# Kernel tuning notes

Measured on AMD Instinct MI355X. Metric: run time of the kernel, lower is better.

Reference implementation:

```python
import jax, jax.numpy as jnp
import numpy as np

D_MODEL = 512
WINDOW = 128
N_HEADS = 8


def setup_inputs() -> dict:
    key = jax.random.key(0)
    k1, k2, k3, k4, k5 = jax.random.split(key, 5)
    B, S, D = 8, 4096, D_MODEL
    scale = 1.0 / np.sqrt(D)
    return {
        "x": jax.random.normal(k1, (B, S, D), dtype=jnp.float32),
        "in_proj_w": jax.random.normal(k2, (3 * D, D), dtype=jnp.float32) * scale,
        "in_proj_b": jax.random.normal(k3, (3 * D,), dtype=jnp.float32) * 0.02,
        "out_proj_w": jax.random.normal(k4, (D, D), dtype=jnp.float32) * scale,
        "out_proj_b": jax.random.normal(k5, (D,), dtype=jnp.float32) * 0.02,
    }


def reference(x, in_proj_w, in_proj_b, out_proj_w, out_proj_b):
    # Non-overlapping sliding-window MHA with shared weights per window.
    B, S, D = x.shape
    W = WINDOW
    H = N_HEADS
    hd = D // H
    nw = S // W  # S chosen divisible by window size

    xw = x.reshape(B, nw, W, D)
    # Fused QKV projection (torch in_proj_weight layout: [3D, D], y = x @ W^T + b)
    qkv = jnp.einsum("bnwd,ed->bnwe", xw, in_proj_w) + in_proj_b  # [B,nw,W,3D]
    q, k, v = jnp.split(qkv, 3, axis=-1)

    def to_heads(t):
        return t.reshape(B, nw, W, H, hd)

    q = to_heads(q) * (1.0 / np.sqrt(hd))
    k = to_heads(k)
    v = to_heads(v)

    # Block-diagonal attention: scores only within each window [B,nw,H,W,W]
    scores = jnp.einsum("bnqhd,bnkhd->bnhqk", q, k)
    attn = jax.nn.softmax(scores, axis=-1)
    ctx = jnp.einsum("bnhqk,bnkhd->bnqhd", attn, v)  # [B,nw,W,H,hd]
    ctx = ctx.reshape(B, S, D)

    out = jnp.einsum("bsd,ed->bse", ctx, out_proj_w) + out_proj_b
    return out
```

## Files before the change

### kernel.cpp

```cpp
#include <hip/hip_runtime.h>


typedef __bf16 bf16x8 __attribute__((ext_vector_type(8)));
typedef __bf16 bf16x4 __attribute__((ext_vector_type(4)));
typedef float  f32x4  __attribute__((ext_vector_type(4)));

#define MFMA16(a, b, c) __builtin_amdgcn_mfma_f32_16x16x32_bf16((a), (b), (c), 0, 0, 0)

#define VMCNT_(n) asm volatile("s_waitcnt vmcnt(" #n ")" ::: "memory")
#define VMCNT(n) VMCNT_(n)
#define LGKM0() asm volatile("s_waitcnt lgkmcnt(0)" ::: "memory")

__device__ __forceinline__ void gload_lds16(const __bf16* g, void* l) {
    __builtin_amdgcn_global_load_lds(
        (const __attribute__((address_space(1))) unsigned int*)g,
        (__attribute__((address_space(3))) unsigned int*)l, 16, 0, 0);
}

__device__ __forceinline__ void cvt8(const float* __restrict__ s,
                                     __bf16* __restrict__ d, long i) {
    const float4* s4 = reinterpret_cast<const float4*>(s);
    float4 a = s4[2 * i], b = s4[2 * i + 1];
    bf16x8 v;
    v[0] = (__bf16)a.x; v[1] = (__bf16)a.y; v[2] = (__bf16)a.z; v[3] = (__bf16)a.w;
    v[4] = (__bf16)b.x; v[5] = (__bf16)b.y; v[6] = (__bf16)b.z; v[7] = (__bf16)b.w;
    *reinterpret_cast<bf16x8*>(d + 8 * i) = v;
}

__global__ void convert_k(const float* __restrict__ x,
                          const float* __restrict__ w_in,
                          const float* __restrict__ w_out,
                          __bf16* __restrict__ x_bf,
                          __bf16* __restrict__ w_in_bf,
                          __bf16* __restrict__ w_out_bf)
{
    long i0 = (long)blockIdx.x * blockDim.x + threadIdx.x;
    long stride = (long)gridDim.x * blockDim.x;
    for (long i = i0; i < 16777216 / 8; i += stride) cvt8(x, x_bf, i);
    for (long i = i0; i < 786432 / 8;   i += stride) cvt8(w_in, w_in_bf, i);
    for (long i = i0; i < 262144 / 8;   i += stride) cvt8(w_out, w_out_bf, i);
}

template<int EPI, int NN>
__global__ __launch_bounds__(512, 2)
void gemm256(const __bf16* __restrict__ A,
             const __bf16* __restrict__ Bw,
             const float* __restrict__ bias,
             void* __restrict__ Cq,
             __bf16* __restrict__ vT)
{
    __shared__ __bf16 Al[4][8192];
    __shared__ __bf16 Bl[4][8192];

    const int nwg = gridDim.x;
    const int chunk = nwg >> 3;
    const int bid = blockIdx.x;
    const int wg = (bid & 7) * chunk + (bid >> 3);
    const int nidx = wg % NN;
    const int midx = wg / NN;
    const long mbase = (long)midx * 256;
    const int colbase = nidx * 256;

    const int tid = threadIdx.x;
    const int w = tid >> 6, lane = tid & 63;
    const int lrow = lane & 15, hi = lane >> 4;
    const int wm = w >> 2, wn = w & 3;

    const int st_row = lane >> 2;
    const int st_k = 8 * ((lane & 3) ^ ((lane >> 3) & 3));
    const int rd_off = 16 * (hi ^ ((lrow >> 1) & 3));

    const __bf16* PA = A  + (mbase + w * 16 + st_row) * 512 + st_k;
    const __bf16* PB = Bw + ((long)colbase + w * 16 + st_row) * 512 + st_k;
    const int lds_w = w * 1024;

    f32x4 acc[8][4];
    #pragma unroll
    for (int rt = 0; rt < 8; ++rt)
        #pragma unroll
        for (int ct = 0; ct < 4; ++ct) acc[rt][ct] = (f32x4){0.f, 0.f, 0.f, 0.f};

    auto stage = [&](int tt) {
        const int kk = tt * 32;
        char* As = (char*)Al[tt & 3];
        char* Bs = (char*)Bl[tt & 3];
        gload_lds16(PA + kk,             As + lds_w);
        gload_lds16(PA + 128 * 512 + kk, As + 8192 + lds_w);
        gload_lds16(PB + kk,             Bs + lds_w);
        gload_lds16(PB + 128 * 512 + kk, Bs + 8192 + lds_w);
    };

#define ITER(T, VM, DO_STG)                                                       \
    {                                                                             \
        VMCNT(VM);                                                                \
        LGKM0();                                                                  \
        __builtin_amdgcn_s_barrier();                                             \
        if (DO_STG) stage((T) + 3);                                               \
        const char* As = (const char*)Al[(T) & 3];                                \
        const char* Bs = (const char*)Bl[(T) & 3];                                \
        bf16x8 af[8], bfr[4];                                                     \
        _Pragma("unroll")                                                         \
        for (int rt = 0; rt < 8; ++rt) {                                          \
            int row = 128 * wm + 16 * rt + lrow;                                  \
            af[rt] = *reinterpret_cast<const bf16x8*>(As + row * 64 + rd_off);    \
        }                                                                         \
        _Pragma("unroll")                                                         \
        for (int ct = 0; ct < 4; ++ct) {                                          \
            int row = 64 * wn + 16 * ct + lrow;                                   \
            bfr[ct] = *reinterpret_cast<const bf16x8*>(Bs + row * 64 + rd_off);   \
        }                                                                         \
        __builtin_amdgcn_s_setprio(1);                                            \
        _Pragma("unroll")                                                         \
        for (int rt = 0; rt < 8; ++rt)                                            \
            _Pragma("unroll")                                                     \
            for (int ct = 0; ct < 4; ++ct)                                        \
                acc[rt][ct] = MFMA16(af[rt], bfr[ct], acc[rt][ct]);               \
        __builtin_amdgcn_s_setprio(0);                                            \
    }

    stage(0); stage(1); stage(2);

    #pragma unroll 1
    for (int t = 0; t < 13; ++t) ITER(t, 8, 1);
    ITER(13, 8, 0);
    ITER(14, 4, 0);
    ITER(15, 0, 0);
#undef ITER

    if (EPI == 0) {
        const int region = colbase >> 9;
        if (region < 2) {
            __bf16* qk = (__bf16*)Cq;
            const float scale = (region == 0) ? 0.125f : 1.0f;
            #pragma unroll
            for (int ct = 0; ct < 4; ++ct) {
                int colg = colbase + 64 * wn + 16 * ct + lrow;
                float b = bias[colg];
                #pragma unroll
                for (int rt = 0; rt < 8; ++rt) {
                    long row = mbase + 128 * wm + 16 * rt + 4 * hi;
                    #pragma unroll
                    for (int r = 0; r < 4; ++r)
                        qk[(row + r) * 1024 + colg] = (__bf16)((acc[rt][ct][r] + b) * scale);
                }
            }
        } else {
            #pragma unroll
            for (int ct = 0; ct < 4; ++ct) {
                int colg = colbase + 64 * wn + 16 * ct + lrow;
                float b = bias[colg];
                int e2 = colg - 1024;
                int h = e2 >> 6, d = e2 & 63;
                #pragma unroll
                for (int rt = 0; rt < 8; ++rt) {
                    long row = mbase + 128 * wm + 16 * rt + 4 * hi;
                    int win = (int)(row >> 7), tok0 = (int)(row & 127);
                    bf16x4 pk;
                    pk[0] = (__bf16)(acc[rt][ct][0] + b);
                    pk[1] = (__bf16)(acc[rt][ct][1] + b);
                    pk[2] = (__bf16)(acc[rt][ct][2] + b);
                    pk[3] = (__bf16)(acc[rt][ct][3] + b);
                    *reinterpret_cast<bf16x4*>(
                        vT + (((long)win * 8 + h) * 64 + d) * 128 + tok0) = pk;
                }
            }
        }
    } else {
        float* out = (float*)Cq;
        #pragma unroll
        for (int ct = 0; ct < 4; ++ct) {
            int colg = colbase + 64 * wn + 16 * ct + lrow;
            float b = bias[colg];
            #pragma unroll
            for (int rt = 0; rt < 8; ++rt) {
                long row = mbase + 128 * wm + 16 * rt + 4 * hi;
                #pragma unroll
                for (int r = 0; r < 4; ++r)
                    out[(row + r) * 512 + colg] = acc[rt][ct][r] + b;
            }
        }
    }
}

__global__ __launch_bounds__(256)
void swa_attn(const __bf16* __restrict__ qk,
              const __bf16* __restrict__ vT,
              __bf16* __restrict__ ctx)
{
    __shared__ __bf16 p_lds[4][32][136];

    const int bid = blockIdx.x;
    const int win = bid >> 3, h = bid & 7;
    const int tid = threadIdx.x;
    const int w = tid >> 6, lane = tid & 63;
    const int lrow = lane & 15, hi = lane >> 4;
    const long tokb = (long)win * 128;

    bf16x8 qa[2][2];
    #pragma unroll
    for (int rt = 0; rt < 2; ++rt)
        #pragma unroll
        for (int ks = 0; ks < 2; ++ks)
            qa[rt][ks] = *reinterpret_cast<const bf16x8*>(
                qk + (tokb + 32 * w + 16 * rt + lrow) * 1024 + h * 64 + ks * 32 + hi * 8);

    f32x4 s[2][8];
    #pragma unroll
    for (int rt = 0; rt < 2; ++rt)
        #pragma unroll
        for (int ct = 0; ct < 8; ++ct) s[rt][ct] = (f32x4){0.f, 0.f, 0.f, 0.f};
    #pragma unroll
    for (int ks = 0; ks < 2; ++ks) {
        #pragma unroll
        for (int ct = 0; ct < 8; ++ct) {
            bf16x8 kb = *reinterpret_cast<const bf16x8*>(
                qk + (tokb + 16 * ct + lrow) * 1024 + 512 + h * 64 + ks * 32 + hi * 8);
            s[0][ct] = MFMA16(qa[0][ks], kb, s[0][ct]);
            s[1][ct] = MFMA16(qa[1][ks], kb, s[1][ct]);
        }
    }

    float inv[2][4];
    #pragma unroll
    for (int rt = 0; rt < 2; ++rt) {
        #pragma unroll
        for (int r = 0; r < 4; ++r) {
            float m = s[rt][0][r];
            #pragma unroll
            for (int ct = 1; ct < 8; ++ct) m = fmaxf(m, s[rt][ct][r]);
            m = fmaxf(m, __shfl_xor(m, 1));
            m = fmaxf(m, __shfl_xor(m, 2));
            m = fmaxf(m, __shfl_xor(m, 4));
            m = fmaxf(m, __shfl_xor(m, 8));
            float sum = 0.f;
            #pragma unroll
            for (int ct = 0; ct < 8; ++ct) {
                float e = __expf(s[rt][ct][r] - m);
                sum += e;
                p_lds[w][16 * rt + 4 * hi + r][16 * ct + lrow] = (__bf16)e;
            }
            sum += __shfl_xor(sum, 1);
            sum += __shfl_xor(sum, 2);
            sum += __shfl_xor(sum, 4);
            sum += __shfl_xor(sum, 8);
            inv[rt][r] = 1.f / sum;
        }
    }

    f32x4 o[2][4];
    #pragma unroll
    for (int rt = 0; rt < 2; ++rt)
        #pragma unroll
        for (int ct = 0; ct < 4; ++ct) o[rt][ct] = (f32x4){0.f, 0.f, 0.f, 0.f};
    const __bf16* vb = vT + ((long)win * 8 + h) * 64 * 128;
    #pragma unroll
    for (int kt = 0; kt < 4; ++kt) {
        bf16x8 pa0 = *reinterpret_cast<const bf16x8*>(&p_lds[w][lrow][32 * kt + 8 * hi]);
        bf16x8 pa1 = *reinterpret_cast<const bf16x8*>(&p_lds[w][16 + lrow][32 * kt + 8 * hi]);
        #pragma unroll
        for (int ct = 0; ct < 4; ++ct) {
            bf16x8 vf = *reinterpret_cast<const bf16x8*>(
                vb + (16 * ct + lrow) * 128 + 32 * kt + 8 * hi);
            o[0][ct] = MFMA16(pa0, vf, o[0][ct]);
            o[1][ct] = MFMA16(pa1, vf, o[1][ct]);
        }
    }

    #pragma unroll
    for (int rt = 0; rt < 2; ++rt)
        #pragma unroll
        for (int ct = 0; ct < 4; ++ct)
            #pragma unroll
            for (int r = 0; r < 4; ++r) {
                long tok = tokb + 32 * w + 16 * rt + 4 * hi + r;
                ctx[tok * 512 + h * 64 + 16 * ct + lrow] =
                    (__bf16)(o[rt][ct][r] * inv[rt][r]);
            }
}

extern "C" void kernel_launch(void* const* d_in, const int* in_sizes, int n_in,
                              void* d_out, int out_size, void* d_ws, size_t ws_size,
                              hipStream_t stream)
{
    const float* x     = (const float*)d_in[0];
    const float* w_in  = (const float*)d_in[1];
    const float* b_in  = (const float*)d_in[2];
    const float* w_out = (const float*)d_in[3];
    const float* b_out = (const float*)d_in[4];

    char* ws = (char*)d_ws;
    __bf16* x_bf     = (__bf16*)(ws);
    __bf16* ctx      = (__bf16*)(ws);
    __bf16* vT       = (__bf16*)(ws + 33554432);
    __bf16* w_in_bf  = (__bf16*)(ws + 67108864);
    __bf16* w_out_bf = (__bf16*)(ws + 68681728);
    __bf16* qk       = (__bf16*)d_out;

    convert_k<<<2048, 256, 0, stream>>>(x, w_in, w_out, x_bf, w_in_bf, w_out_bf);
    gemm256<0, 6><<<768, 512, 0, stream>>>(x_bf, w_in_bf, b_in, (void*)qk, vT);
    swa_attn<<<2048, 256, 0, stream>>>(qk, vT, ctx);
    gemm256<1, 2><<<256, 512, 0, stream>>>(ctx, w_out_bf, b_out, d_out, nullptr);
}
```

Measured before the change: 176.3 us.

## Restructure GEMM to BK=64 double-buffered pipeline with LDS-staged coalesced epilogues

Reworks the 256x256 GEMM main loop: K tiles grow from 32 to 64 with two LDS buffers instead of four. Each tile is split into four barrier-separated sub-phases that reuse the B fragments across A row groups, with a new XOR swizzle layout. All epilogues now stage results through LDS so global writes to qk, the transposed vT and the fp32 output are 16-byte coalesced vectors. This trades extra barriers and less prefetch depth (one tile ahead, then full vmcnt(0) waits) for fewer loop iterations, fewer registers and better store coalescing.

```diff
diff --git a/kernel.cpp b/kernel.cpp
--- a/kernel.cpp
+++ b/kernel.cpp
@@ -2,7 +2,6 @@
 
 
 typedef __bf16 bf16x8 __attribute__((ext_vector_type(8)));
-typedef __bf16 bf16x4 __attribute__((ext_vector_type(4)));
 typedef float  f32x4  __attribute__((ext_vector_type(4)));
 
 #define MFMA16(a, b, c) __builtin_amdgcn_mfma_f32_16x16x32_bf16((a), (b), (c), 0, 0, 0)
@@ -49,8 +48,7 @@
              void* __restrict__ Cq,
              __bf16* __restrict__ vT)
 {
-    __shared__ __bf16 Al[4][8192];
-    __shared__ __bf16 Bl[4][8192];
+    __shared__ __align__(16) char smem[131072];
 
     const int nwg = gridDim.x;
     const int chunk = nwg >> 3;
@@ -64,15 +62,28 @@
     const int tid = threadIdx.x;
     const int w = tid >> 6, lane = tid & 63;
     const int lrow = lane & 15, hi = lane >> 4;
+    const int quad = lane >> 4, sl = lane & 15;
     const int wm = w >> 2, wn = w & 3;
 
-    const int st_row = lane >> 2;
-    const int st_k = 8 * ((lane & 3) ^ ((lane >> 3) & 3));
-    const int rd_off = 16 * (hi ^ ((lrow >> 1) & 3));
-
-    const __bf16* PA = A  + (mbase + w * 16 + st_row) * 512 + st_k;
-    const __bf16* PB = Bw + ((long)colbase + w * 16 + st_row) * 512 + st_k;
-    const int lds_w = w * 1024;
+    const int l8 = lane >> 3;
+    const int slotp = (lane & 7) ^ l8;
+    const __bf16* stA = A  + (mbase + 8 * w + l8) * 512 + slotp * 8;
+    const __bf16* stB = Bw + ((long)colbase + 8 * w + l8) * 512 + slotp * 8;
+    const int ldsw = w * 1024;
+
+    auto stage8 = [&](int tt) {
+        char* As = smem + (tt & 1) * 32768;
+        char* Bs = smem + 65536 + (tt & 1) * 32768;
+        const int ko = tt * 64;
+        gload_lds16(stA + ko,             As + ldsw);
+        gload_lds16(stA + 64 * 512 + ko,  As + 8192 + ldsw);
+        gload_lds16(stA + 128 * 512 + ko, As + 16384 + ldsw);
+        gload_lds16(stA + 192 * 512 + ko, As + 24576 + ldsw);
+        gload_lds16(stB + ko,             Bs + ldsw);
+        gload_lds16(stB + 64 * 512 + ko,  Bs + 8192 + ldsw);
+        gload_lds16(stB + 128 * 512 + ko, Bs + 16384 + ldsw);
+        gload_lds16(stB + 192 * 512 + ko, Bs + 24576 + ldsw);
+    };
 
     f32x4 acc[8][4];
     #pragma unroll
@@ -80,104 +91,152 @@
         #pragma unroll
         for (int ct = 0; ct < 4; ++ct) acc[rt][ct] = (f32x4){0.f, 0.f, 0.f, 0.f};
 
-    auto stage = [&](int tt) {
-        const int kk = tt * 32;
-        char* As = (char*)Al[tt & 3];
-        char* Bs = (char*)Bl[tt & 3];
-        gload_lds16(PA + kk,             As + lds_w);
-        gload_lds16(PA + 128 * 512 + kk, As + 8192 + lds_w);
-        gload_lds16(PB + kk,             Bs + lds_w);
-        gload_lds16(PB + 128 * 512 + kk, Bs + 8192 + lds_w);
-    };
-
-#define ITER(T, VM, DO_STG)                                                       \
+    bf16x8 af[4], bfr[4];
+
+#define PHASE(T, KK, RT0, LB)                                                     \
     {                                                                             \
-        VMCNT(VM);                                                                \
-        LGKM0();                                                                  \
-        __builtin_amdgcn_s_barrier();                                             \
-        if (DO_STG) stage((T) + 3);                                               \
-        const char* As = (const char*)Al[(T) & 3];                                \
-        const char* Bs = (const char*)Bl[(T) & 3];                                \
-        bf16x8 af[8], bfr[4];                                                     \
-        _Pragma("unroll")                                                         \
-        for (int rt = 0; rt < 8; ++rt) {                                          \
-            int row = 128 * wm + 16 * rt + lrow;                                  \
-            af[rt] = *reinterpret_cast<const bf16x8*>(As + row * 64 + rd_off);    \
+        const char* As = smem + ((T) & 1) * 32768;                                \
+        const char* Bs = smem + 65536 + ((T) & 1) * 32768;                        \
+        const int ko = ((KK) * 64 + hi * 16) ^ ((lrow & 7) << 4);                 \
+        if (LB) {                                                                 \
+            _Pragma("unroll")                                                     \
+            for (int ct = 0; ct < 4; ++ct)                                        \
+                bfr[ct] = *reinterpret_cast<const bf16x8*>(                       \
+                    Bs + (64 * wn + 16 * ct + lrow) * 128 + ko);                  \
         }                                                                         \
         _Pragma("unroll")                                                         \
-        for (int ct = 0; ct < 4; ++ct) {                                          \
-            int row = 64 * wn + 16 * ct + lrow;                                   \
-            bfr[ct] = *reinterpret_cast<const bf16x8*>(Bs + row * 64 + rd_off);   \
-        }                                                                         \
+        for (int i = 0; i < 4; ++i)                                               \
+            af[i] = *reinterpret_cast<const bf16x8*>(                             \
+                As + (128 * wm + 16 * ((RT0) + i) + lrow) * 128 + ko);            \
         __builtin_amdgcn_s_setprio(1);                                            \
         _Pragma("unroll")                                                         \
-        for (int rt = 0; rt < 8; ++rt)                                            \
+        for (int i = 0; i < 4; ++i)                                               \
             _Pragma("unroll")                                                     \
             for (int ct = 0; ct < 4; ++ct)                                        \
-                acc[rt][ct] = MFMA16(af[rt], bfr[ct], acc[rt][ct]);               \
+                acc[(RT0) + i][ct] = MFMA16(af[i], bfr[ct], acc[(RT0) + i][ct]);  \
         __builtin_amdgcn_s_setprio(0);                                            \
     }
 
-    stage(0); stage(1); stage(2);
+    stage8(0); stage8(1);
+    VMCNT(8);
+    __builtin_amdgcn_s_barrier();
 
     #pragma unroll 1
-    for (int t = 0; t < 13; ++t) ITER(t, 8, 1);
-    ITER(13, 8, 0);
-    ITER(14, 4, 0);
-    ITER(15, 0, 0);
-#undef ITER
-
+    for (int t = 0; t < 8; ++t) {
+        if (t) {
+            VMCNT(0);
+            __builtin_amdgcn_s_barrier();
+            if (t < 7) stage8(t + 1);
+        }
+        PHASE(t, 0, 0, 1);
+        __builtin_amdgcn_s_barrier();
+        PHASE(t, 0, 4, 0);
+        __builtin_amdgcn_s_barrier();
+        PHASE(t, 1, 0, 1);
+        __builtin_amdgcn_s_barrier();
+        PHASE(t, 1, 4, 0);
+    }
+#undef PHASE
+    __builtin_amdgcn_s_barrier();
+
+    const int colg0 = colbase + 64 * wn + lrow;
     if (EPI == 0) {
-        const int region = colbase >> 9;
-        if (region < 2) {
+        if (colbase < 1024) {
+            const float scale = (colbase < 512) ? 0.125f : 1.0f;
             __bf16* qk = (__bf16*)Cq;
-            const float scale = (region == 0) ? 0.125f : 1.0f;
             #pragma unroll
             for (int ct = 0; ct < 4; ++ct) {
-                int colg = colbase + 64 * wn + 16 * ct + lrow;
-                float b = bias[colg];
-                #pragma unroll
-                for (int rt = 0; rt < 8; ++rt) {
-                    long row = mbase + 128 * wm + 16 * rt + 4 * hi;
+                float b = bias[colg0 + 16 * ct];
+                int col2 = (64 * wn + 16 * ct + lrow) * 2;
+                #pragma unroll
+                for (int rt = 0; rt < 8; ++rt)
                     #pragma unroll
-                    for (int r = 0; r < 4; ++r)
-                        qk[(row + r) * 1024 + colg] = (__bf16)((acc[rt][ct][r] + b) * scale);
+                    for (int r = 0; r < 4; ++r) {
+                        int row = 128 * wm + 16 * rt + 4 * hi + r;
+                        *reinterpret_cast<__bf16*>(
+                            smem + row * 512 + (col2 ^ ((row & 31) << 4))) =
+                            (__bf16)((acc[rt][ct][r] + b) * scale);
+                    }
+            }
+            LGKM0();
+            __builtin_amdgcn_s_barrier();
+            #pragma unroll
+            for (int i = 0; i < 8; ++i) {
+                int row = 32 * w + 4 * i + quad;
+                #pragma unroll
+                for (int h2 = 0; h2 < 2; ++h2) {
+                    int slot = (16 * h2 + sl) ^ (row & 31);
+                    bf16x8 v = *reinterpret_cast<const bf16x8*>(smem + row * 512 + slot * 16);
+                    *reinterpret_cast<bf16x8*>(
+                        qk + (mbase + row) * 1024 + colbase + h2 * 128 + sl * 8) = v;
                 }
             }
         } else {
             #pragma unroll
             for (int ct = 0; ct < 4; ++ct) {
-                int colg = colbase + 64 * wn + 16 * ct + lrow;
-                float b = bias[colg];
-                int e2 = colg - 1024;
-                int h = e2 >> 6, d = e2 & 63;
-                #pragma unroll
-                for (int rt = 0; rt < 8; ++rt) {
-                    long row = mbase + 128 * wm + 16 * rt + 4 * hi;
-                    int win = (int)(row >> 7), tok0 = (int)(row & 127);
-                    bf16x4 pk;
-                    pk[0] = (__bf16)(acc[rt][ct][0] + b);
-                    pk[1] = (__bf16)(acc[rt][ct][1] + b);
-                    pk[2] = (__bf16)(acc[rt][ct][2] + b);
-                    pk[3] = (__bf16)(acc[rt][ct][3] + b);
-                    *reinterpret_cast<bf16x4*>(
-                        vT + (((long)win * 8 + h) * 64 + d) * 128 + tok0) = pk;
+                float b = bias[colg0 + 16 * ct];
+                int e = 64 * wn + 16 * ct + lrow;
+                #pragma unroll
+                for (int rt = 0; rt < 8; ++rt)
+                    #pragma unroll
+                    for (int r = 0; r < 4; ++r) {
+                        int tok = 128 * wm + 16 * rt + 4 * hi + r;
+                        *reinterpret_cast<__bf16*>(
+                            smem + e * 512 + ((tok * 2) ^ ((e & 31) << 4))) =
+                            (__bf16)(acc[rt][ct][r] + b);
+                    }
+            }
+            LGKM0();
+            __builtin_amdgcn_s_barrier();
+            #pragma unroll
+            for (int i = 0; i < 8; ++i) {
+                int e = 32 * w + 4 * i + quad;
+                #pragma unroll
+                for (int h2 = 0; h2 < 2; ++h2) {
+                    int slot = (16 * h2 + sl) ^ (e & 31);
+                    bf16x8 v = *reinterpret_cast<const bf16x8*>(smem + e * 512 + slot * 16);
+                    *reinterpret_cast<bf16x8*>(
+                        vT + (long)(2 * midx + h2) * 65536 +
+                        (colbase - 1024 + e) * 128 + sl * 8) = v;
                 }
             }
         }
     } else {
-        float* out = (float*)Cq;
-        #pragma unroll
-        for (int ct = 0; ct < 4; ++ct) {
-            int colg = colbase + 64 * wn + 16 * ct + lrow;
-            float b = bias[colg];
-            #pragma unroll
-            for (int rt = 0; rt < 8; ++rt) {
-                long row = mbase + 128 * wm + 16 * rt + 4 * hi;
-                #pragma unroll
-                for (int r = 0; r < 4; ++r)
-                    out[(row + r) * 512 + colg] = acc[rt][ct][r] + b;
-            }
+        float* outp = (float*)Cq;
+        float bb[4];
+        #pragma unroll
+        for (int ct = 0; ct < 4; ++ct) bb[ct] = bias[colg0 + 16 * ct];
+        #pragma unroll 1
+        for (int half = 0; half < 2; ++half) {
+            if (wm == half) {
+                #pragma unroll
+                for (int ct = 0; ct < 4; ++ct) {
+                    int c4 = (64 * wn + 16 * ct + lrow) * 4;
+                    #pragma unroll
+                    for (int rt = 0; rt < 8; ++rt)
+                        #pragma unroll
+                        for (int r = 0; r < 4; ++r) {
+                            int row = 16 * rt + 4 * hi + r;
+                            *reinterpret_cast<float*>(
+                                smem + row * 1024 + (c4 ^ ((row & 63) << 4))) =
+                                acc[rt][ct][r] + bb[ct];
+                        }
+                }
+            }
+            LGKM0();
+            __builtin_amdgcn_s_barrier();
+            #pragma unroll
+            for (int i = 0; i < 4; ++i) {
+                int row = 16 * w + 4 * i + quad;
+                #pragma unroll
+                for (int h2 = 0; h2 < 4; ++h2) {
+                    int slot = (16 * h2 + sl) ^ (row & 63);
+                    f32x4 v = *reinterpret_cast<const f32x4*>(smem + row * 1024 + slot * 16);
+                    *reinterpret_cast<f32x4*>(
+                        outp + (mbase + 128 * half + row) * 512 + colbase + h2 * 64 + sl * 4) = v;
+                }
+            }
+            __builtin_amdgcn_s_barrier();
         }
     }
 }
```

After: 177.2 us. No clear change (+0.5%).
